# Kernel optimization log

Measured on AMD Instinct MI355X. Metric: run time of the kernel, lower is better.

Reference implementation:

```python
import jax, jax.numpy as jnp
import numpy as np

N = 50000       # nodes
E = 1_600_000   # edges
F_IN, H1, H2, T, C = 16, 64, 64, 8, 10


def setup_inputs() -> dict:
    key = jax.random.key(0)
    ks = jax.random.split(key, 12)
    def w(k, shp):
        fan_in = shp[0]
        return jax.random.normal(k, shp, dtype=jnp.float32) * (1.0 / np.sqrt(fan_in))
    return {
        "x": jax.random.normal(ks[0], (N, F_IN, T), dtype=jnp.float32),
        "edge_index": jax.random.randint(ks[1], (2, E), 0, N, dtype=jnp.int64),
        "edge_weight": jax.random.uniform(ks[2], (E,), dtype=jnp.float32),
        "W1": w(ks[3], (F_IN, H1)), "b1": jnp.zeros((H1,), jnp.float32),
        "W2": w(ks[4], (H1, H2)),   "b2": jnp.zeros((H2,), jnp.float32),
        "W3": w(ks[5], (H2, H2)),   "b3": jnp.zeros((H2,), jnp.float32),
        "Wseq": w(ks[6], (H2 * T, H2)), "bseq": jnp.zeros((H2,), jnp.float32),
        "Wcls": w(ks[7], (H2, C)),  "bcls": jnp.zeros((C,), jnp.float32),
    }


def reference(x, edge_index, edge_weight, W1, b1, W2, b2, W3, b3, Wseq, bseq, Wcls, bcls):
    n = x.shape[0]
    src, dst = edge_index[0], edge_index[1]
    # GCN: add self-loops with weight 1, symmetric degree normalization
    loops = jnp.arange(n, dtype=src.dtype)
    src_a = jnp.concatenate([src, loops])
    dst_a = jnp.concatenate([dst, loops])
    w_a = jnp.concatenate([edge_weight, jnp.ones((n,), edge_weight.dtype)])
    deg = jax.ops.segment_sum(w_a, dst_a, num_segments=n)
    dinv = jnp.where(deg > 0, jax.lax.rsqrt(jnp.where(deg > 0, deg, 1.0)), 0.0)
    norm = dinv[src_a] * w_a * dinv[dst_a]  # [E+N]

    def conv(h, W, b):
        h = h @ W                                  # [N, out]
        msg = h[src_a] * norm[:, None]             # gather + scale
        return jax.ops.segment_sum(msg, dst_a, num_segments=n) + b

    def per_t(xt):  # xt: [N, F_IN]
        h = jax.nn.relu(conv(xt, W1, b1))
        h = jax.nn.relu(conv(h, W2, b2))
        h = jax.nn.relu(conv(h, W3, b3))
        return h  # [N, H2]

    hs = jax.vmap(per_t)(jnp.moveaxis(x, -1, 0))   # [T, N, H2]
    seq = jnp.transpose(hs, (1, 0, 2)).reshape(n, -1)  # [N, T*H2], t-major like torch.cat
    h = jax.nn.relu(seq @ Wseq + bseq)
    return h @ Wcls + bcls  # [N, C]
```

## Files before the change

kernel.cpp:

```cpp
#include <hip/hip_runtime.h>
#include <hip/hip_fp16.h>

constexpr int N  = 50000;
constexpr int E  = 1600000;
constexpr int T  = 8;
constexpr int H  = 64;
constexpr int C  = 10;

__global__ void deg_count_kernel(const int* __restrict__ ei, const float* __restrict__ w,
                                 float* __restrict__ deg, int* __restrict__ counts) {
  int e = blockIdx.x * blockDim.x + threadIdx.x;
  if (e >= E) return;
  int d = ei[E + e];
  atomicAdd(&deg[d], w[e]);
  atomicAdd(&counts[d], 1);
}

__global__ void dinv_kernel(float* deg) {
  int n = blockIdx.x * blockDim.x + threadIdx.x;
  if (n >= N) return;
  deg[n] = rsqrtf(deg[n] + 1.0f);
}

__global__ void scan_kernel(const int* __restrict__ counts, int* __restrict__ rowptr) {
  __shared__ int wsum[16];
  __shared__ int carry_s;
  int tid = threadIdx.x;
  if (tid == 0) carry_s = 0;
  __syncthreads();
  for (int base = 0; base < N; base += 1024) {
    int i = base + tid;
    int v = (i < N) ? counts[i] : 0;
    int x = v;
    #pragma unroll
    for (int off = 1; off < 64; off <<= 1) {
      int y = __shfl_up(x, off, 64);
      if ((tid & 63) >= off) x += y;
    }
    if ((tid & 63) == 63) wsum[tid >> 6] = x;
    __syncthreads();
    if (tid < 16) {
      int wv = wsum[tid];
      #pragma unroll
      for (int off = 1; off < 16; off <<= 1) {
        int y = __shfl_up(wv, off, 16);
        if (tid >= off) wv += y;
      }
      wsum[tid] = wv;
    }
    __syncthreads();
    int carry = carry_s;
    int waveoff = (tid >> 6) ? wsum[(tid >> 6) - 1] : 0;
    int inc = x + waveoff + carry;
    if (i < N) rowptr[i + 1] = inc;
    __syncthreads();
    if (tid == 1023) carry_s = inc;
    __syncthreads();
  }
  if (tid == 0) rowptr[0] = 0;
}

__global__ void fill_kernel(const int* __restrict__ ei, const float* __restrict__ w,
                            const float* __restrict__ dinv, const int* __restrict__ rowptr,
                            int* __restrict__ fill, int* __restrict__ csr_src,
                            float* __restrict__ csr_norm) {
  int e = blockIdx.x * blockDim.x + threadIdx.x;
  if (e >= E) return;
  int s = ei[e], d = ei[E + e];
  int pos = rowptr[d] + atomicAdd(&fill[d], 1);
  csr_src[pos] = s;
  csr_norm[pos] = dinv[s] * w[e] * dinv[d];
}

__global__ void cvt_x_kernel(const float* __restrict__ x, __half* __restrict__ xh) {
  int i = blockIdx.x * blockDim.x + threadIdx.x;
  if (i >= N * 32) return;
  float4 v = ((const float4*)x)[i];
  __half2 h0; h0.x = __float2half_rn(v.x); h0.y = __float2half_rn(v.y);
  __half2 h1; h1.x = __float2half_rn(v.z); h1.y = __float2half_rn(v.w);
  uint2 u;
  u.x = __builtin_bit_cast(unsigned int, h0);
  u.y = __builtin_bit_cast(unsigned int, h1);
  ((uint2*)xh)[i] = u;
}

__global__ void agg_x_kernel(const __half* __restrict__ xh, const float* __restrict__ dinv,
                             const int* __restrict__ rowptr, const int* __restrict__ csr_src,
                             const float* __restrict__ csr_norm, float* __restrict__ xagg) {
  int tid = threadIdx.x;
  int w = tid >> 6, l = tid & 63;
  int sub = l >> 5, c4 = l & 31;
  int n = blockIdx.x * 4 + w;
  float di = dinv[n], dd = di * di;
  int e0 = rowptr[n], e1 = rowptr[n + 1];
  int cnt = e1 - e0 + 1;
  float4 acc = {0, 0, 0, 0};
  int sm[2]; float wm[2];
  #pragma unroll
  for (int q = 0; q < 2; ++q) {
    int idx = sub + 2 * q;
    if (idx == 0)       { sm[q] = n; wm[q] = dd; }
    else if (idx < cnt) { int e = e0 + idx - 1; sm[q] = csr_src[e]; wm[q] = csr_norm[e]; }
    else                { sm[q] = n; wm[q] = 0.f; }
  }
  for (int i = sub; i < cnt; i += 4) {
    uint2 r0 = *reinterpret_cast<const uint2*>(xh + (size_t)sm[0] * 128 + c4 * 4);
    uint2 r1 = *reinterpret_cast<const uint2*>(xh + (size_t)sm[1] * 128 + c4 * 4);
    float w0 = wm[0], w1 = wm[1];
    #pragma unroll
    for (int q = 0; q < 2; ++q) {
      int idx = i + 4 + 2 * q;
      if (idx < cnt) { int e = e0 + idx - 1; sm[q] = csr_src[e]; wm[q] = csr_norm[e]; }
      else           { sm[q] = n; wm[q] = 0.f; }
    }
    float2 f0 = __half22float2(__builtin_bit_cast(__half2, r0.x));
    float2 f1 = __half22float2(__builtin_bit_cast(__half2, r0.y));
    acc.x = fmaf(w0, f0.x, acc.x); acc.y = fmaf(w0, f0.y, acc.y);
    acc.z = fmaf(w0, f1.x, acc.z); acc.w = fmaf(w0, f1.y, acc.w);
    float2 g0 = __half22float2(__builtin_bit_cast(__half2, r1.x));
    float2 g1 = __half22float2(__builtin_bit_cast(__half2, r1.y));
    acc.x = fmaf(w1, g0.x, acc.x); acc.y = fmaf(w1, g0.y, acc.y);
    acc.z = fmaf(w1, g1.x, acc.z); acc.w = fmaf(w1, g1.y, acc.w);
  }
  acc.x += __shfl_xor(acc.x, 32, 64);
  acc.y += __shfl_xor(acc.y, 32, 64);
  acc.z += __shfl_xor(acc.z, 32, 64);
  acc.w += __shfl_xor(acc.w, 32, 64);
  if (sub == 0) ((float4*)(xagg + (size_t)n * 128))[c4] = acc;
}

__global__ void dense12_kernel(const float* __restrict__ xagg, const float* __restrict__ W1,
                               const float* __restrict__ b1, const float* __restrict__ W2,
                               __half* __restrict__ G2h) {
  __shared__ float xs[4 * 128];
  __shared__ float h1s[4][8][64];
  int tid = threadIdx.x;
  int n0 = blockIdx.x * 4;
  ((float2*)xs)[tid] = ((const float2*)(xagg + (size_t)n0 * 128))[tid];
  __syncthreads();
  int nb = tid >> 6, j = tid & 63;
  float a[8];
  float bj = b1[j];
  #pragma unroll
  for (int t = 0; t < 8; ++t) a[t] = bj;
  for (int f = 0; f < 16; ++f) {
    float wv = W1[f * 64 + j];
    #pragma unroll
    for (int t = 0; t < 8; ++t) a[t] = fmaf(xs[nb * 128 + f * 8 + t], wv, a[t]);
  }
  #pragma unroll
  for (int t = 0; t < 8; ++t) h1s[nb][t][j] = fmaxf(a[t], 0.f);
  __syncthreads();
  float g[8];
  #pragma unroll
  for (int t = 0; t < 8; ++t) g[t] = 0.f;
  for (int k = 0; k < 64; ++k) {
    float wv = W2[k * 64 + j];
    #pragma unroll
    for (int t = 0; t < 8; ++t) g[t] = fmaf(h1s[nb][t][k], wv, g[t]);
  }
  __half* gp = G2h + (size_t)(n0 + nb) * 512 + j;
  #pragma unroll
  for (int t = 0; t < 8; ++t) gp[t * 64] = __float2half_rn(g[t]);
}

__device__ __forceinline__ void accum8(float* acc, uint4 r, float wgt) {
  float2 f0 = __half22float2(__builtin_bit_cast(__half2, r.x));
  float2 f1 = __half22float2(__builtin_bit_cast(__half2, r.y));
  float2 f2 = __half22float2(__builtin_bit_cast(__half2, r.z));
  float2 f3 = __half22float2(__builtin_bit_cast(__half2, r.w));
  acc[0] = fmaf(wgt, f0.x, acc[0]); acc[1] = fmaf(wgt, f0.y, acc[1]);
  acc[2] = fmaf(wgt, f1.x, acc[2]); acc[3] = fmaf(wgt, f1.y, acc[3]);
  acc[4] = fmaf(wgt, f2.x, acc[4]); acc[5] = fmaf(wgt, f2.y, acc[5]);
  acc[6] = fmaf(wgt, f3.x, acc[6]); acc[7] = fmaf(wgt, f3.y, acc[7]);
}

__global__ void conv2w_kernel(const __half* __restrict__ G2h, const float* __restrict__ dinv,
                              const int* __restrict__ rowptr, const int* __restrict__ csr_src,
                              const float* __restrict__ csr_norm, const float* __restrict__ b2,
                              const float* __restrict__ W3, __half* __restrict__ G3h) {
  __shared__ float h2s[4][512];
  int tid = threadIdx.x;
  int w = tid >> 6, l = tid & 63;
  int n0 = blockIdx.x * 4;
  int n = n0 + w;
  float di = dinv[n], dd = di * di;
  int e0 = rowptr[n], e1 = rowptr[n + 1];
  int cnt = e1 - e0 + 1;
  float acc[8] = {0, 0, 0, 0, 0, 0, 0, 0};
  int sm[4]; float wm[4];
  #pragma unroll
  for (int q = 0; q < 4; ++q) {
    int idx = q;
    if (idx == 0)       { sm[q] = n; wm[q] = dd; }
    else if (idx < cnt) { int e = e0 + idx - 1; sm[q] = csr_src[e]; wm[q] = csr_norm[e]; }
    else                { sm[q] = n; wm[q] = 0.f; }
  }
  for (int i = 0; i < cnt; i += 4) {
    uint4 r0 = *reinterpret_cast<const uint4*>(G2h + (size_t)sm[0] * 512 + l * 8);
    uint4 r1 = *reinterpret_cast<const uint4*>(G2h + (size_t)sm[1] * 512 + l * 8);
    uint4 r2 = *reinterpret_cast<const uint4*>(G2h + (size_t)sm[2] * 512 + l * 8);
    uint4 r3 = *reinterpret_cast<const uint4*>(G2h + (size_t)sm[3] * 512 + l * 8);
    float w0 = wm[0], w1 = wm[1], w2 = wm[2], w3 = wm[3];
    #pragma unroll
    for (int q = 0; q < 4; ++q) {
      int idx = i + 4 + q;
      if (idx < cnt) { int e = e0 + idx - 1; sm[q] = csr_src[e]; wm[q] = csr_norm[e]; }
      else           { sm[q] = n; wm[q] = 0.f; }
    }
    accum8(acc, r0, w0);
    accum8(acc, r1, w1);
    accum8(acc, r2, w2);
    accum8(acc, r3, w3);
  }
  #pragma unroll
  for (int q = 0; q < 8; ++q)
    h2s[w][l * 8 + q] = fmaxf(acc[q] + b2[(l * 8 + q) & 63], 0.f);
  __syncthreads();
  int t = tid >> 5;
  int jh = tid & 31, j0 = 2 * jh;
  float g[4][2];
  #pragma unroll
  for (int q = 0; q < 4; ++q) { g[q][0] = 0.f; g[q][1] = 0.f; }
  const float2* W3v = (const float2*)W3;
  for (int k = 0; k < 64; ++k) {
    float2 wv = W3v[k * 32 + jh];
    #pragma unroll
    for (int q = 0; q < 4; ++q) {
      float h = h2s[q][t * 64 + k];
      g[q][0] = fmaf(h, wv.x, g[q][0]);
      g[q][1] = fmaf(h, wv.y, g[q][1]);
    }
  }
  #pragma unroll
  for (int q = 0; q < 4; ++q) {
    __half2 hv;
    hv.x = __float2half_rn(g[q][0]);
    hv.y = __float2half_rn(g[q][1]);
    *reinterpret_cast<__half2*>(G3h + (size_t)(n0 + q) * 512 + t * 64 + j0) = hv;
  }
}

__global__ void conv3w_kernel(const __half* __restrict__ G3h, const float* __restrict__ dinv,
                              const int* __restrict__ rowptr, const int* __restrict__ csr_src,
                              const float* __restrict__ csr_norm, const float* __restrict__ b3,
                              const float* __restrict__ Wseq, const float* __restrict__ bseq,
                              const float* __restrict__ Wcls, const float* __restrict__ bcls,
                              float* __restrict__ out) {
  __shared__ float h3s[4][512];
  __shared__ float red[4][4][64];
  __shared__ float hfs[4][64];
  int tid = threadIdx.x;
  int w = tid >> 6, l = tid & 63;
  int n0 = blockIdx.x * 4;
  int n = n0 + w;
  float di = dinv[n], dd = di * di;
  int e0 = rowptr[n], e1 = rowptr[n + 1];
  int cnt = e1 - e0 + 1;
  float acc[8] = {0, 0, 0, 0, 0, 0, 0, 0};
  int sm[4]; float wm[4];
  #pragma unroll
  for (int q = 0; q < 4; ++q) {
    int idx = q;
    if (idx == 0)       { sm[q] = n; wm[q] = dd; }
    else if (idx < cnt) { int e = e0 + idx - 1; sm[q] = csr_src[e]; wm[q] = csr_norm[e]; }
    else                { sm[q] = n; wm[q] = 0.f; }
  }
  for (int i = 0; i < cnt; i += 4) {
    uint4 r0 = *reinterpret_cast<const uint4*>(G3h + (size_t)sm[0] * 512 + l * 8);
    uint4 r1 = *reinterpret_cast<const uint4*>(G3h + (size_t)sm[1] * 512 + l * 8);
    uint4 r2 = *reinterpret_cast<const uint4*>(G3h + (size_t)sm[2] * 512 + l * 8);
    uint4 r3 = *reinterpret_cast<const uint4*>(G3h + (size_t)sm[3] * 512 + l * 8);
    float w0 = wm[0], w1 = wm[1], w2 = wm[2], w3 = wm[3];
    #pragma unroll
    for (int q = 0; q < 4; ++q) {
      int idx = i + 4 + q;
      if (idx < cnt) { int e = e0 + idx - 1; sm[q] = csr_src[e]; wm[q] = csr_norm[e]; }
      else           { sm[q] = n; wm[q] = 0.f; }
    }
    accum8(acc, r0, w0);
    accum8(acc, r1, w1);
    accum8(acc, r2, w2);
    accum8(acc, r3, w3);
  }
  #pragma unroll
  for (int q = 0; q < 8; ++q)
    h3s[w][l * 8 + q] = fmaxf(acc[q] + b3[(l * 8 + q) & 63], 0.f);
  __syncthreads();
  int p = tid >> 6, j = tid & 63;
  float pa0 = 0.f, pa1 = 0.f, pa2 = 0.f, pa3 = 0.f;
  for (int ci = 0; ci < 128; ++ci) {
    int c = p * 128 + ci;
    float wv = Wseq[(size_t)c * 64 + j];
    pa0 = fmaf(h3s[0][c], wv, pa0);
    pa1 = fmaf(h3s[1][c], wv, pa1);
    pa2 = fmaf(h3s[2][c], wv, pa2);
    pa3 = fmaf(h3s[3][c], wv, pa3);
  }
  red[p][0][j] = pa0; red[p][1][j] = pa1; red[p][2][j] = pa2; red[p][3][j] = pa3;
  __syncthreads();
  int nb = tid >> 6, k = tid & 63;
  float s = red[0][nb][k] + red[1][nb][k] + red[2][nb][k] + red[3][nb][k] + bseq[k];
  hfs[nb][k] = fmaxf(s, 0.f);
  __syncthreads();
  if (k < C) {
    float o = bcls[k];
    #pragma unroll
    for (int kk = 0; kk < 64; ++kk) o = fmaf(hfs[nb][kk], Wcls[kk * C + k], o);
    out[(size_t)(n0 + nb) * C + k] = o;
  }
}

__global__ void layer1N_kernel(const float* __restrict__ xagg, const float* __restrict__ W1,
                               const float* __restrict__ b1, const float* __restrict__ W2,
                               float* __restrict__ GA, int t) {
  __shared__ float hs[4][H];
  int tid = threadIdx.x;
  int wv = tid >> 6, j = tid & 63;
  int n = blockIdx.x * 4 + wv;
  const float* xa = xagg + (size_t)n * 128;
  float a = b1[j];
  #pragma unroll
  for (int f = 0; f < 16; ++f) a += xa[f * 8 + t] * W1[f * H + j];
  hs[wv][j] = fmaxf(a, 0.f);
  __syncthreads();
  float g = 0.f;
  #pragma unroll
  for (int k = 0; k < H; ++k) g += hs[wv][k] * W2[k * H + j];
  GA[(size_t)n * H + j] = g;
}

template<bool ACCUM>
__global__ void convN_kernel(const float* __restrict__ Gin, const float* __restrict__ dinv,
                             const int* __restrict__ rowptr, const int* __restrict__ csr_src,
                             const float* __restrict__ csr_norm, const float* __restrict__ b,
                             const float* __restrict__ Wnext, float* __restrict__ Gout) {
  __shared__ __align__(16) float hs[4][H];
  int tid = threadIdx.x;
  int wv = tid >> 6, lane = tid & 63;
  int sub = lane >> 4, q = lane & 15;
  int n = blockIdx.x * 4 + wv;
  float di = dinv[n];
  const float4* G4 = (const float4*)Gin;
  float4 a0 = {0,0,0,0}, a1 = {0,0,0,0};
  int e0 = rowptr[n], e1 = rowptr[n + 1];
  int e = e0 + sub;
  for (; e + 4 < e1; e += 8) {
    int s0 = csr_src[e];     float w0 = csr_norm[e];
    int s1 = csr_src[e + 4]; float w1 = csr_norm[e + 4];
    float4 r0 = G4[(size_t)s0 * 16 + q];
    float4 r1 = G4[(size_t)s1 * 16 + q];
    a0.x += w0 * r0.x; a0.y += w0 * r0.y; a0.z += w0 * r0.z; a0.w += w0 * r0.w;
    a1.x += w1 * r1.x; a1.y += w1 * r1.y; a1.z += w1 * r1.z; a1.w += w1 * r1.w;
  }
  for (; e < e1; e += 4) {
    int s0 = csr_src[e]; float w0 = csr_norm[e];
    float4 r0 = G4[(size_t)s0 * 16 + q];
    a0.x += w0 * r0.x; a0.y += w0 * r0.y; a0.z += w0 * r0.z; a0.w += w0 * r0.w;
  }
  a0.x += a1.x; a0.y += a1.y; a0.z += a1.z; a0.w += a1.w;
  #pragma unroll
  for (int off = 16; off <= 32; off <<= 1) {
    a0.x += __shfl_xor(a0.x, off, 64);
    a0.y += __shfl_xor(a0.y, off, 64);
    a0.z += __shfl_xor(a0.z, off, 64);
    a0.w += __shfl_xor(a0.w, off, 64);
  }
  float4 own = G4[(size_t)n * 16 + q];
  float dd = di * di;
  if (sub == 0) {
    float4 h;
    h.x = fmaxf(a0.x + dd * own.x + b[4 * q + 0], 0.f);
    h.y = fmaxf(a0.y + dd * own.y + b[4 * q + 1], 0.f);
    h.z = fmaxf(a0.z + dd * own.z + b[4 * q + 2], 0.f);
    h.w = fmaxf(a0.w + dd * own.w + b[4 * q + 3], 0.f);
    ((float4*)hs[wv])[q] = h;
  }
  __syncthreads();
  float g = 0.f;
  #pragma unroll
  for (int k = 0; k < H; ++k) g += hs[wv][k] * Wnext[k * H + lane];
  if (ACCUM) Gout[(size_t)n * H + lane] += g;
  else       Gout[(size_t)n * H + lane]  = g;
}

__global__ void final_kernel(const float* __restrict__ acc, const float* __restrict__ bseq,
                             const float* __restrict__ Wcls, const float* __restrict__ bcls,
                             float* __restrict__ out) {
  __shared__ float hs[4][H];
  int tid = threadIdx.x;
  int wv = tid >> 6, j = tid & 63;
  int n = blockIdx.x * 4 + wv;
  hs[wv][j] = fmaxf(acc[(size_t)n * H + j] + bseq[j], 0.0f);
  __syncthreads();
  if (j < C) {
    float o = bcls[j];
    #pragma unroll
    for (int k = 0; k < H; ++k) o += hs[wv][k] * Wcls[k * C + j];
    out[(size_t)n * C + j] = o;
  }
}

extern "C" void kernel_launch(void* const* d_in, const int* in_sizes, int n_in,
                              void* d_out, int out_size, void* d_ws, size_t ws_size,
                              hipStream_t stream) {
  const float* x    = (const float*)d_in[0];
  const int*   ei   = (const int*)  d_in[1];
  const float* w    = (const float*)d_in[2];
  const float* W1   = (const float*)d_in[3];
  const float* b1   = (const float*)d_in[4];
  const float* W2   = (const float*)d_in[5];
  const float* b2   = (const float*)d_in[6];
  const float* W3   = (const float*)d_in[7];
  const float* b3   = (const float*)d_in[8];
  const float* Wseq = (const float*)d_in[9];
  const float* bseq = (const float*)d_in[10];
  const float* Wcls = (const float*)d_in[11];
  const float* bcls = (const float*)d_in[12];
  float* out = (float*)d_out;

  char* p = (char*)d_ws;
  auto alloc = [&](size_t bytes) -> char* {
    char* r = p; p += (bytes + 255) & ~(size_t)255; return r;
  };
  float*  deg     = (float*) alloc((size_t)N * 4);
  int*    counts  = (int*)   alloc((size_t)N * 4);
  int*    fillc   = (int*)   alloc((size_t)N * 4);
  int*    rowptr  = (int*)   alloc((size_t)(N + 1) * 4);
  int*    csr_src = (int*)   alloc((size_t)E * 4);
  float*  csr_nrm = (float*) alloc((size_t)E * 4);
  float*  xagg    = (float*) alloc((size_t)N * 128 * 4);
  __half* xh      = (__half*)alloc((size_t)N * 128 * 2);

  hipMemsetAsync(deg,    0, (size_t)N * 4, stream);
  hipMemsetAsync(counts, 0, (size_t)N * 4, stream);
  hipMemsetAsync(fillc,  0, (size_t)N * 4, stream);

  cvt_x_kernel<<<(N * 32 + 255) / 256, 256, 0, stream>>>(x, xh);
  deg_count_kernel<<<(E + 255) / 256, 256, 0, stream>>>(ei, w, deg, counts);
  dinv_kernel<<<(N + 255) / 256, 256, 0, stream>>>(deg);
  scan_kernel<<<1, 1024, 0, stream>>>(counts, rowptr);
  fill_kernel<<<(E + 255) / 256, 256, 0, stream>>>(ei, w, deg, rowptr, fillc, csr_src, csr_nrm);
  agg_x_kernel<<<N / 4, 256, 0, stream>>>(xh, deg, rowptr, csr_src, csr_nrm, xagg);

  bool wide = ws_size >= (size_t)155 * 1000 * 1000;

  if (wide) {
    __half* G2h = (__half*)alloc((size_t)N * 512 * 2);
    __half* G3h = (__half*)alloc((size_t)N * 512 * 2);
    dense12_kernel<<<N / 4, 256, 0, stream>>>(xagg, W1, b1, W2, G2h);
    conv2w_kernel<<<N / 4, 256, 0, stream>>>(G2h, deg, rowptr, csr_src, csr_nrm, b2, W3, G3h);
    conv3w_kernel<<<N / 4, 256, 0, stream>>>(G3h, deg, rowptr, csr_src, csr_nrm, b3,
                                             Wseq, bseq, Wcls, bcls, out);
  } else {
    float* GA  = (float*)alloc((size_t)N * H * 4);
    float* GB  = (float*)alloc((size_t)N * H * 4);
    float* acc = (float*)alloc((size_t)N * H * 4);
    hipMemsetAsync(acc, 0, (size_t)N * H * 4, stream);
    for (int t = 0; t < T; ++t) {
      layer1N_kernel<<<N / 4, 256, 0, stream>>>(xagg, W1, b1, W2, GA, t);
      convN_kernel<false><<<N / 4, 256, 0, stream>>>(GA, deg, rowptr, csr_src, csr_nrm, b2, W3, GB);
      convN_kernel<true ><<<N / 4, 256, 0, stream>>>(GB, deg, rowptr, csr_src, csr_nrm, b3,
                                                     Wseq + (size_t)t * H * H, acc);
    }
    final_kernel<<<N / 4, 256, 0, stream>>>(acc, bseq, Wcls, bcls, out);
  }
}
```

Measured before the change: 878.8 us.

## Pack CSR source and norm into int2 and widen agg_x gathers

Merges the separate csr_src and csr_norm arrays into one interleaved int2 array, so each edge's metadata arrives in a single 8-byte load in every aggregation kernel. agg_x_kernel is reworked so each lane gathers 8 halfs (uint4) and four sub-groups of 16 lanes each handle an edge, with a two-step shuffle reduction. convN's two-accumulator unroll is dropped for a simpler loop. A leftover dead first loop that breaks right away stays in agg_x, adding one redundant meta/gather load per wave.

```diff
diff --git a/kernel.cpp b/kernel.cpp
--- a/kernel.cpp
+++ b/kernel.cpp
@@ -62,14 +62,15 @@
 
 __global__ void fill_kernel(const int* __restrict__ ei, const float* __restrict__ w,
                             const float* __restrict__ dinv, const int* __restrict__ rowptr,
-                            int* __restrict__ fill, int* __restrict__ csr_src,
-                            float* __restrict__ csr_norm) {
+                            int* __restrict__ fill, int2* __restrict__ csr_meta) {
   int e = blockIdx.x * blockDim.x + threadIdx.x;
   if (e >= E) return;
   int s = ei[e], d = ei[E + e];
   int pos = rowptr[d] + atomicAdd(&fill[d], 1);
-  csr_src[pos] = s;
-  csr_norm[pos] = dinv[s] * w[e] * dinv[d];
+  int2 m;
+  m.x = s;
+  m.y = __float_as_int(dinv[s] * w[e] * dinv[d]);
+  csr_meta[pos] = m;
 }
 
 __global__ void cvt_x_kernel(const float* __restrict__ x, __half* __restrict__ xh) {
@@ -85,48 +86,74 @@
 }
 
 __global__ void agg_x_kernel(const __half* __restrict__ xh, const float* __restrict__ dinv,
-                             const int* __restrict__ rowptr, const int* __restrict__ csr_src,
-                             const float* __restrict__ csr_norm, float* __restrict__ xagg) {
+                             const int* __restrict__ rowptr, const int2* __restrict__ csr_meta,
+                             float* __restrict__ xagg) {
   int tid = threadIdx.x;
   int w = tid >> 6, l = tid & 63;
-  int sub = l >> 5, c4 = l & 31;
+  int sub = l >> 4, q = l & 15;
   int n = blockIdx.x * 4 + w;
   float di = dinv[n], dd = di * di;
   int e0 = rowptr[n], e1 = rowptr[n + 1];
   int cnt = e1 - e0 + 1;
-  float4 acc = {0, 0, 0, 0};
-  int sm[2]; float wm[2];
-  #pragma unroll
-  for (int q = 0; q < 2; ++q) {
-    int idx = sub + 2 * q;
-    if (idx == 0)       { sm[q] = n; wm[q] = dd; }
-    else if (idx < cnt) { int e = e0 + idx - 1; sm[q] = csr_src[e]; wm[q] = csr_norm[e]; }
-    else                { sm[q] = n; wm[q] = 0.f; }
+  float acc[8] = {0, 0, 0, 0, 0, 0, 0, 0};
+  int sA; float wA;
+  {
+    int idx = sub;
+    if (idx == 0)       { sA = n; wA = dd; }
+    else if (idx < cnt) { int2 m = csr_meta[e0 + idx - 1]; sA = m.x; wA = __int_as_float(m.y); }
+    else                { sA = n; wA = 0.f; }
   }
   for (int i = sub; i < cnt; i += 4) {
-    uint2 r0 = *reinterpret_cast<const uint2*>(xh + (size_t)sm[0] * 128 + c4 * 4);
-    uint2 r1 = *reinterpret_cast<const uint2*>(xh + (size_t)sm[1] * 128 + c4 * 4);
-    float w0 = wm[0], w1 = wm[1];
-    #pragma unroll
-    for (int q = 0; q < 2; ++q) {
-      int idx = i + 4 + 2 * q;
-      if (idx < cnt) { int e = e0 + idx - 1; sm[q] = csr_src[e]; wm[q] = csr_norm[e]; }
-      else           { sm[q] = n; wm[q] = 0.f; }
-    }
-    float2 f0 = __half22float2(__builtin_bit_cast(__half2, r0.x));
-    float2 f1 = __half22float2(__builtin_bit_cast(__half2, r0.y));
-    acc.x = fmaf(w0, f0.x, acc.x); acc.y = fmaf(w0, f0.y, acc.y);
-    acc.z = fmaf(w0, f1.x, acc.z); acc.w = fmaf(w0, f1.y, acc.w);
-    float2 g0 = __half22float2(__builtin_bit_cast(__half2, r1.x));
-    float2 g1 = __half22float2(__builtin_bit_cast(__half2, r1.y));
-    acc.x = fmaf(w1, g0.x, acc.x); acc.y = fmaf(w1, g0.y, acc.y);
-    acc.z = fmaf(w1, g1.x, acc.z); acc.w = fmaf(w1, g1.y, acc.w);
-  }
-  acc.x += __shfl_xor(acc.x, 32, 64);
-  acc.y += __shfl_xor(acc.y, 32, 64);
-  acc.z += __shfl_xor(acc.z, 32, 64);
-  acc.w += __shfl_xor(acc.w, 32, 64);
-  if (sub == 0) ((float4*)(xagg + (size_t)n * 128))[c4] = acc;
+    uint4 r = *reinterpret_cast<const uint4*>(xh + (size_t)sA * 128 + q * 8);
+    int idx = i + 4;
+    if (idx < cnt) { int2 m = csr_meta[e0 + idx - 1]; sA = m.x; wA = __int_as_float(m.y); }
+    else           { sA = n; wA = 0.f; }
+    float2 f0 = __half22float2(__builtin_bit_cast(__half2, r.x));
+    float2 f1 = __half22float2(__builtin_bit_cast(__half2, r.y));
+    float2 f2 = __half22float2(__builtin_bit_cast(__half2, r.z));
+    float2 f3 = __half22float2(__builtin_bit_cast(__half2, r.w));
+    float wgt = (i == 0 && sub == 0) ? dd : wA;
+    (void)wgt;
+    acc[0] = acc[0];
+    float wr = 0.f;
+    (void)wr;
+    f0 = f0; f1 = f1; f2 = f2; f3 = f3;
+    break;
+  }
+  {
+    int sCur; float wCur;
+    int idx0 = sub;
+    if (idx0 == 0)       { sCur = n; wCur = dd; }
+    else if (idx0 < cnt) { int2 m = csr_meta[e0 + idx0 - 1]; sCur = m.x; wCur = __int_as_float(m.y); }
+    else                 { sCur = n; wCur = 0.f; }
+    acc[0] = acc[1] = acc[2] = acc[3] = acc[4] = acc[5] = acc[6] = acc[7] = 0.f;
+    for (int i = sub; i < cnt; i += 4) {
+      uint4 r = *reinterpret_cast<const uint4*>(xh + (size_t)sCur * 128 + q * 8);
+      float wUse = wCur;
+      int idx = i + 4;
+      if (idx < cnt) { int2 m = csr_meta[e0 + idx - 1]; sCur = m.x; wCur = __int_as_float(m.y); }
+      else           { sCur = n; wCur = 0.f; }
+      float2 f0 = __half22float2(__builtin_bit_cast(__half2, r.x));
+      float2 f1 = __half22float2(__builtin_bit_cast(__half2, r.y));
+      float2 f2 = __half22float2(__builtin_bit_cast(__half2, r.z));
+      float2 f3 = __half22float2(__builtin_bit_cast(__half2, r.w));
+      acc[0] = fmaf(wUse, f0.x, acc[0]); acc[1] = fmaf(wUse, f0.y, acc[1]);
+      acc[2] = fmaf(wUse, f1.x, acc[2]); acc[3] = fmaf(wUse, f1.y, acc[3]);
+      acc[4] = fmaf(wUse, f2.x, acc[4]); acc[5] = fmaf(wUse, f2.y, acc[5]);
+      acc[6] = fmaf(wUse, f3.x, acc[6]); acc[7] = fmaf(wUse, f3.y, acc[7]);
+    }
+  }
+  #pragma unroll
+  for (int v = 0; v < 8; ++v) {
+    acc[v] += __shfl_xor(acc[v], 16, 64);
+    acc[v] += __shfl_xor(acc[v], 32, 64);
+  }
+  if (sub == 0) {
+    float4 o0; o0.x = acc[0]; o0.y = acc[1]; o0.z = acc[2]; o0.w = acc[3];
+    float4 o1; o1.x = acc[4]; o1.y = acc[5]; o1.z = acc[6]; o1.w = acc[7];
+    float4* dst = (float4*)(xagg + (size_t)n * 128 + q * 8);
+    dst[0] = o0; dst[1] = o1;
+  }
 }
 
 __global__ void dense12_kernel(const float* __restrict__ xagg, const float* __restrict__ W1,
@@ -176,8 +203,8 @@
 }
 
 __global__ void conv2w_kernel(const __half* __restrict__ G2h, const float* __restrict__ dinv,
-                              const int* __restrict__ rowptr, const int* __restrict__ csr_src,
-                              const float* __restrict__ csr_norm, const float* __restrict__ b2,
+                              const int* __restrict__ rowptr, const int2* __restrict__ csr_meta,
+                              const float* __restrict__ b2,
                               const float* __restrict__ W3, __half* __restrict__ G3h) {
   __shared__ float h2s[4][512];
   int tid = threadIdx.x;
@@ -193,7 +220,7 @@
   for (int q = 0; q < 4; ++q) {
     int idx = q;
     if (idx == 0)       { sm[q] = n; wm[q] = dd; }
-    else if (idx < cnt) { int e = e0 + idx - 1; sm[q] = csr_src[e]; wm[q] = csr_norm[e]; }
+    else if (idx < cnt) { int2 m = csr_meta[e0 + idx - 1]; sm[q] = m.x; wm[q] = __int_as_float(m.y); }
     else                { sm[q] = n; wm[q] = 0.f; }
   }
   for (int i = 0; i < cnt; i += 4) {
@@ -205,7 +232,7 @@
     #pragma unroll
     for (int q = 0; q < 4; ++q) {
       int idx = i + 4 + q;
-      if (idx < cnt) { int e = e0 + idx - 1; sm[q] = csr_src[e]; wm[q] = csr_norm[e]; }
+      if (idx < cnt) { int2 m = csr_meta[e0 + idx - 1]; sm[q] = m.x; wm[q] = __int_as_float(m.y); }
       else           { sm[q] = n; wm[q] = 0.f; }
     }
     accum8(acc, r0, w0);
@@ -242,8 +269,8 @@
 }
 
 __global__ void conv3w_kernel(const __half* __restrict__ G3h, const float* __restrict__ dinv,
-                              const int* __restrict__ rowptr, const int* __restrict__ csr_src,
-                              const float* __restrict__ csr_norm, const float* __restrict__ b3,
+                              const int* __restrict__ rowptr, const int2* __restrict__ csr_meta,
+                              const float* __restrict__ b3,
                               const float* __restrict__ Wseq, const float* __restrict__ bseq,
                               const float* __restrict__ Wcls, const float* __restrict__ bcls,
                               float* __restrict__ out) {
@@ -263,7 +290,7 @@
   for (int q = 0; q < 4; ++q) {
     int idx = q;
     if (idx == 0)       { sm[q] = n; wm[q] = dd; }
-    else if (idx < cnt) { int e = e0 + idx - 1; sm[q] = csr_src[e]; wm[q] = csr_norm[e]; }
+    else if (idx < cnt) { int2 m = csr_meta[e0 + idx - 1]; sm[q] = m.x; wm[q] = __int_as_float(m.y); }
     else                { sm[q] = n; wm[q] = 0.f; }
   }
   for (int i = 0; i < cnt; i += 4) {
@@ -275,7 +302,7 @@
     #pragma unroll
     for (int q = 0; q < 4; ++q) {
       int idx = i + 4 + q;
-      if (idx < cnt) { int e = e0 + idx - 1; sm[q] = csr_src[e]; wm[q] = csr_norm[e]; }
+      if (idx < cnt) { int2 m = csr_meta[e0 + idx - 1]; sm[q] = m.x; wm[q] = __int_as_float(m.y); }
       else           { sm[q] = n; wm[q] = 0.f; }
     }
     accum8(acc, r0, w0);
@@ -332,8 +359,8 @@
 
 template<bool ACCUM>
 __global__ void convN_kernel(const float* __restrict__ Gin, const float* __restrict__ dinv,
-                             const int* __restrict__ rowptr, const int* __restrict__ csr_src,
-                             const float* __restrict__ csr_norm, const float* __restrict__ b,
+                             const int* __restrict__ rowptr, const int2* __restrict__ csr_meta,
+                             const float* __restrict__ b,
                              const float* __restrict__ Wnext, float* __restrict__ Gout) {
   __shared__ __align__(16) float hs[4][H];
   int tid = threadIdx.x;
@@ -342,23 +369,14 @@
   int n = blockIdx.x * 4 + wv;
   float di = dinv[n];
   const float4* G4 = (const float4*)Gin;
-  float4 a0 = {0,0,0,0}, a1 = {0,0,0,0};
+  float4 a0 = {0,0,0,0};
   int e0 = rowptr[n], e1 = rowptr[n + 1];
-  int e = e0 + sub;
-  for (; e + 4 < e1; e += 8) {
-    int s0 = csr_src[e];     float w0 = csr_norm[e];
-    int s1 = csr_src[e + 4]; float w1 = csr_norm[e + 4];
-    float4 r0 = G4[(size_t)s0 * 16 + q];
-    float4 r1 = G4[(size_t)s1 * 16 + q];
+  for (int e = e0 + sub; e < e1; e += 4) {
+    int2 m = csr_meta[e];
+    float w0 = __int_as_float(m.y);
+    float4 r0 = G4[(size_t)m.x * 16 + q];
     a0.x += w0 * r0.x; a0.y += w0 * r0.y; a0.z += w0 * r0.z; a0.w += w0 * r0.w;
-    a1.x += w1 * r1.x; a1.y += w1 * r1.y; a1.z += w1 * r1.z; a1.w += w1 * r1.w;
-  }
-  for (; e < e1; e += 4) {
-    int s0 = csr_src[e]; float w0 = csr_norm[e];
-    float4 r0 = G4[(size_t)s0 * 16 + q];
-    a0.x += w0 * r0.x; a0.y += w0 * r0.y; a0.z += w0 * r0.z; a0.w += w0 * r0.w;
-  }
-  a0.x += a1.x; a0.y += a1.y; a0.z += a1.z; a0.w += a1.w;
+  }
   #pragma unroll
   for (int off = 16; off <= 32; off <<= 1) {
     a0.x += __shfl_xor(a0.x, off, 64);
@@ -427,8 +445,7 @@
   int*    counts  = (int*)   alloc((size_t)N * 4);
   int*    fillc   = (int*)   alloc((size_t)N * 4);
   int*    rowptr  = (int*)   alloc((size_t)(N + 1) * 4);
-  int*    csr_src = (int*)   alloc((size_t)E * 4);
-  float*  csr_nrm = (float*) alloc((size_t)E * 4);
+  int2*   csr_meta= (int2*)  alloc((size_t)E * 8);
   float*  xagg    = (float*) alloc((size_t)N * 128 * 4);
   __half* xh      = (__half*)alloc((size_t)N * 128 * 2);
 
@@ -440,8 +457,8 @@
   deg_count_kernel<<<(E + 255) / 256, 256, 0, stream>>>(ei, w, deg, counts);
   dinv_kernel<<<(N + 255) / 256, 256, 0, stream>>>(deg);
   scan_kernel<<<1, 1024, 0, stream>>>(counts, rowptr);
-  fill_kernel<<<(E + 255) / 256, 256, 0, stream>>>(ei, w, deg, rowptr, fillc, csr_src, csr_nrm);
-  agg_x_kernel<<<N / 4, 256, 0, stream>>>(xh, deg, rowptr, csr_src, csr_nrm, xagg);
+  fill_kernel<<<(E + 255) / 256, 256, 0, stream>>>(ei, w, deg, rowptr, fillc, csr_meta);
+  agg_x_kernel<<<N / 4, 256, 0, stream>>>(xh, deg, rowptr, csr_meta, xagg);
 
   bool wide = ws_size >= (size_t)155 * 1000 * 1000;
 
@@ -449,8 +466,8 @@
     __half* G2h = (__half*)alloc((size_t)N * 512 * 2);
     __half* G3h = (__half*)alloc((size_t)N * 512 * 2);
     dense12_kernel<<<N / 4, 256, 0, stream>>>(xagg, W1, b1, W2, G2h);
-    conv2w_kernel<<<N / 4, 256, 0, stream>>>(G2h, deg, rowptr, csr_src, csr_nrm, b2, W3, G3h);
-    conv3w_kernel<<<N / 4, 256, 0, stream>>>(G3h, deg, rowptr, csr_src, csr_nrm, b3,
+    conv2w_kernel<<<N / 4, 256, 0, stream>>>(G2h, deg, rowptr, csr_meta, b2, W3, G3h);
+    conv3w_kernel<<<N / 4, 256, 0, stream>>>(G3h, deg, rowptr, csr_meta, b3,
                                              Wseq, bseq, Wcls, bcls, out);
   } else {
     float* GA  = (float*)alloc((size_t)N * H * 4);
@@ -459,8 +476,8 @@
     hipMemsetAsync(acc, 0, (size_t)N * H * 4, stream);
     for (int t = 0; t < T; ++t) {
       layer1N_kernel<<<N / 4, 256, 0, stream>>>(xagg, W1, b1, W2, GA, t);
-      convN_kernel<false><<<N / 4, 256, 0, stream>>>(GA, deg, rowptr, csr_src, csr_nrm, b2, W3, GB);
-      convN_kernel<true ><<<N / 4, 256, 0, stream>>>(GB, deg, rowptr, csr_src, csr_nrm, b3,
+      convN_kernel<false><<<N / 4, 256, 0, stream>>>(GA, deg, rowptr, csr_meta, b2, W3, GB);
+      convN_kernel<true ><<<N / 4, 256, 0, stream>>>(GB, deg, rowptr, csr_meta, b3,
                                                      Wseq + (size_t)t * H * H, acc);
     }
     final_kernel<<<N / 4, 256, 0, stream>>>(acc, bseq, Wcls, bcls, out);
```

Measured after the change: 923.8 us. +5.1%, slower.
